# Optimization experiments

Hardware: AMD Instinct MI355X
Metric: run time of the kernel (lower is better)

## Reference

```python
import jax, jax.numpy as jnp
import numpy as np

ITER_ROUTING = 3
SIZE_IN_CAPS = 8


def squash(s, axis=-1):
    sq = jnp.sum(s * s, axis=axis, keepdims=True)
    # scale = ||s||^2 / (1 + ||s||^2); then divide by ||s|| (faithful to torch code)
    return (sq / (1.0 + sq)) * s / jnp.sqrt(sq)


def setup_inputs() -> dict:
    key = jax.random.key(0)
    k1, k2 = jax.random.split(key)
    x = jax.random.normal(k1, (256, 32, 8, 6, 6), dtype=jnp.float32)
    W = jax.random.normal(k2, (1, 10, 1152, 16, 8), dtype=jnp.float32)
    return {"x": x, "W": W}


def reference(x, W):
    B = x.shape[0]
    # torch: x.reshape(B,1,-1,8,1); W @ x -> [B,10,1152,16,1] -> squeeze
    xr = x.reshape(B, -1, SIZE_IN_CAPS)          # [B, in_caps, 8]
    u = jnp.einsum('hiws,bis->bhiw', W[0], xr)   # [B, 10, 1152, 16]
    b = jnp.zeros(u.shape[:3] + (1,), dtype=u.dtype)  # routing logits
    v = None
    for _ in range(ITER_ROUTING):
        c = jax.nn.softmax(b, axis=-2)           # softmax over in_caps
        s = jnp.sum(u * c, axis=-2)              # [B, 10, 16]
        v = squash(s, axis=-1)
        agreement = jnp.sum(u * v[:, :, None, :], axis=-1, keepdims=True)
        b = b + agreement
    return v
```

## Files before the change

### kernel.cpp

```cpp
#include <hip/hip_runtime.h>
#include <math.h>

#define NB 256
#define NH 10
#define NI 1152
#define NW 16
#define NS 8


__global__ __launch_bounds__(512, 2)
void digitcaps_kernel(const float* __restrict__ x,
                      const float* __restrict__ Wc,
                      float* __restrict__ out)
{
    __shared__ float u_lds[2][NW * NI];
    __shared__ float e_lds[2][NI];
    __shared__ float redM[8];
    __shared__ float redE[8];
    __shared__ float red3[8][16];
    __shared__ float vacc_sh[2][16];

    const int tid  = threadIdx.x;
    const int half = tid >> 8;
    const int t    = tid & 255;
    const int w    = t & 15;
    const int il   = t >> 4;
    const int lane = tid & 63;
    const int wid  = tid >> 6;

    const int blk = blockIdx.x;
    const int h   = blk >> 7;
    const int bg  = blk & 127;
    const int b   = bg * 2 + half;

    const float* xb = x  + (size_t)b * (NI * NS);
    const float* Wh = Wc + (size_t)h * ((size_t)NI * NW * NS);

    float u_reg[72];

    #pragma unroll
    for (int k = 0; k < 72; ++k) {
        int i = k * 16 + il;
        const float4* xp = reinterpret_cast<const float4*>(xb + (size_t)i * NS);
        float4 x0 = xp[0], x1 = xp[1];
        const float4* wp = reinterpret_cast<const float4*>(Wh + ((size_t)i * NW + w) * NS);
        float4 w0 = wp[0], w1 = wp[1];
        float a = w0.x*x0.x + w0.y*x0.y + w0.z*x0.z + w0.w*x0.w
                + w1.x*x1.x + w1.y*x1.y + w1.z*x1.z + w1.w*x1.w;
        u_reg[k] = a;
        u_lds[half][w * NI + (i ^ (2 * w))] = a;
    }
    if (tid < 32) vacc_sh[tid >> 4][tid & 15] = 0.0f;
    __syncthreads();

    for (int r = 0; r < 3; ++r) {
        if (r > 0) {
            float vloc[16];
            #pragma unroll
            for (int q = 0; q < 16; ++q) vloc[q] = vacc_sh[half][q];
            float dk[5];
            float m = -3.4e38f;
            #pragma unroll
            for (int k = 0; k < 5; ++k) {
                int i = t + 256 * k;
                if (k < 4 || t < (NI - 1024)) {
                    float d = 0.0f;
                    #pragma unroll
                    for (int q = 0; q < 16; ++q)
                        d += u_lds[half][q * NI + (i ^ (2 * q))] * vloc[q];
                    dk[k] = d;
                    m = fmaxf(m, d);
                }
            }
            #pragma unroll
            for (int s = 1; s < 64; s <<= 1) m = fmaxf(m, __shfl_xor(m, s));
            if (lane == 0) redM[wid] = m;
            __syncthreads();
            float M = fmaxf(fmaxf(redM[half*4+0], redM[half*4+1]),
                            fmaxf(redM[half*4+2], redM[half*4+3]));
            float Es = 0.0f;
            #pragma unroll
            for (int k = 0; k < 5; ++k) {
                int i = t + 256 * k;
                if (k < 4 || t < (NI - 1024)) {
                    float e = __expf(dk[k] - M);
                    e_lds[half][i] = e;
                    Es += e;
                }
            }
            #pragma unroll
            for (int s = 1; s < 64; s <<= 1) Es += __shfl_xor(Es, s);
            if (lane == 0) redE[wid] = Es;
            __syncthreads();
        }
        float acc = 0.0f;
        if (r == 0) {
            #pragma unroll
            for (int k = 0; k < 72; ++k) acc += u_reg[k];
        } else {
            #pragma unroll
            for (int k = 0; k < 72; ++k) acc += e_lds[half][k * 16 + il] * u_reg[k];
        }
        acc += __shfl_xor(acc, 16);
        acc += __shfl_xor(acc, 32);
        if (lane < 16) red3[wid][lane] = acc;
        __syncthreads();
        if (tid < 32) {
            int hh = tid >> 4, w2 = tid & 15;
            float s = red3[hh*4+0][w2] + red3[hh*4+1][w2]
                    + red3[hh*4+2][w2] + red3[hh*4+3][w2];
            float Eh = (r == 0) ? (float)NI
                     : (redE[hh*4+0] + redE[hh*4+1] + redE[hh*4+2] + redE[hh*4+3]);
            s /= Eh;
            float sq = s * s;
            #pragma unroll
            for (int st = 1; st < 16; st <<= 1) sq += __shfl_xor(sq, st);
            float f = sqrtf(sq) / (1.0f + sq);
            float v = s * f;
            if (r < 2) vacc_sh[hh][w2] += v;
            else {
                int bb = bg * 2 + hh;
                out[((size_t)bb * NH + h) * NW + w2] = v;
            }
        }
        __syncthreads();
    }
}

extern "C" void kernel_launch(void* const* d_in, const int* in_sizes, int n_in,
                              void* d_out, int out_size, void* d_ws, size_t ws_size,
                              hipStream_t stream) {
    const float* x  = (const float*)d_in[0];
    const float* Wc = (const float*)d_in[1];
    float* out = (float*)d_out;
    digitcaps_kernel<<<dim3(1280), dim3(512), 0, stream>>>(x, Wc, out);
}
```

Baseline: 171.8 us.

## Keep full u tile in registers with 4-lane DPP agreement and fused softmax

Each thread now holds 4 output dimensions for 18 input capsules, with one batch per 256-thread block. The agreement dot product is reduced across 4 lanes with DPP adds instead of reading a 72 KB LDS copy of u. The softmax drops max subtraction and fuses exp, normalizer and weighted sum into one pass. This removes the large shared-memory footprint, the LDS round trips and several barriers, allowing more blocks per CU. The cost is more registers per thread, and skipping max subtraction risks exp overflow for large agreement values.

```diff
diff --git a/kernel.cpp b/kernel.cpp
--- a/kernel.cpp
+++ b/kernel.cpp
@@ -1,127 +1,109 @@
 #include <hip/hip_runtime.h>
 #include <math.h>
 
-#define NB 256
 #define NH 10
 #define NI 1152
 #define NW 16
 #define NS 8
+#define NK 18
 
+template<int CTRL>
+__device__ __forceinline__ float dpp_add(float v) {
+    union { float f; int i; } a, r;
+    a.f = v;
+    r.i = __builtin_amdgcn_update_dpp(a.i, a.i, CTRL, 0xF, 0xF, true);
+    return v + r.f;
+}
 
-__global__ __launch_bounds__(512, 2)
+__global__ __launch_bounds__(256, 4)
 void digitcaps_kernel(const float* __restrict__ x,
                       const float* __restrict__ Wc,
                       float* __restrict__ out)
 {
-    __shared__ float u_lds[2][NW * NI];
-    __shared__ float e_lds[2][NI];
-    __shared__ float redM[8];
-    __shared__ float redE[8];
-    __shared__ float red3[8][16];
-    __shared__ float vacc_sh[2][16];
+    __shared__ float red3[4][NW];
+    __shared__ float redE[4];
+    __shared__ float vacc_sh[NW];
 
     const int tid  = threadIdx.x;
-    const int half = tid >> 8;
-    const int t    = tid & 255;
-    const int w    = t & 15;
-    const int il   = t >> 4;
+    const int wq   = tid & 3;
+    const int il   = tid >> 2;
     const int lane = tid & 63;
     const int wid  = tid >> 6;
 
-    const int blk = blockIdx.x;
-    const int h   = blk >> 7;
-    const int bg  = blk & 127;
-    const int b   = bg * 2 + half;
+    const int h = blockIdx.x >> 8;
+    const int b = blockIdx.x & 255;
 
     const float* xb = x  + (size_t)b * (NI * NS);
     const float* Wh = Wc + (size_t)h * ((size_t)NI * NW * NS);
 
-    float u_reg[72];
+    float u[4][NK];
 
     #pragma unroll
-    for (int k = 0; k < 72; ++k) {
-        int i = k * 16 + il;
+    for (int k = 0; k < NK; ++k) {
+        const int i = k * 64 + il;
         const float4* xp = reinterpret_cast<const float4*>(xb + (size_t)i * NS);
-        float4 x0 = xp[0], x1 = xp[1];
-        const float4* wp = reinterpret_cast<const float4*>(Wh + ((size_t)i * NW + w) * NS);
-        float4 w0 = wp[0], w1 = wp[1];
-        float a = w0.x*x0.x + w0.y*x0.y + w0.z*x0.z + w0.w*x0.w
-                + w1.x*x1.x + w1.y*x1.y + w1.z*x1.z + w1.w*x1.w;
-        u_reg[k] = a;
-        u_lds[half][w * NI + (i ^ (2 * w))] = a;
+        const float4 x0 = xp[0], x1 = xp[1];
+        #pragma unroll
+        for (int j = 0; j < 4; ++j) {
+            const float4* wp = reinterpret_cast<const float4*>(
+                Wh + ((size_t)i * NW + 4 * j + wq) * NS);
+            const float4 w0 = wp[0], w1 = wp[1];
+            u[j][k] = w0.x*x0.x + w0.y*x0.y + w0.z*x0.z + w0.w*x0.w
+                    + w1.x*x1.x + w1.y*x1.y + w1.z*x1.z + w1.w*x1.w;
+        }
     }
-    if (tid < 32) vacc_sh[tid >> 4][tid & 15] = 0.0f;
-    __syncthreads();
 
     for (int r = 0; r < 3; ++r) {
-        if (r > 0) {
-            float vloc[16];
-            #pragma unroll
-            for (int q = 0; q < 16; ++q) vloc[q] = vacc_sh[half][q];
-            float dk[5];
-            float m = -3.4e38f;
-            #pragma unroll
-            for (int k = 0; k < 5; ++k) {
-                int i = t + 256 * k;
-                if (k < 4 || t < (NI - 1024)) {
-                    float d = 0.0f;
-                    #pragma unroll
-                    for (int q = 0; q < 16; ++q)
-                        d += u_lds[half][q * NI + (i ^ (2 * q))] * vloc[q];
-                    dk[k] = d;
-                    m = fmaxf(m, d);
-                }
-            }
-            #pragma unroll
-            for (int s = 1; s < 64; s <<= 1) m = fmaxf(m, __shfl_xor(m, s));
-            if (lane == 0) redM[wid] = m;
-            __syncthreads();
-            float M = fmaxf(fmaxf(redM[half*4+0], redM[half*4+1]),
-                            fmaxf(redM[half*4+2], redM[half*4+3]));
-            float Es = 0.0f;
-            #pragma unroll
-            for (int k = 0; k < 5; ++k) {
-                int i = t + 256 * k;
-                if (k < 4 || t < (NI - 1024)) {
-                    float e = __expf(dk[k] - M);
-                    e_lds[half][i] = e;
-                    Es += e;
-                }
-            }
-            #pragma unroll
-            for (int s = 1; s < 64; s <<= 1) Es += __shfl_xor(Es, s);
-            if (lane == 0) redE[wid] = Es;
-            __syncthreads();
-        }
-        float acc = 0.0f;
+        float acc0 = 0.f, acc1 = 0.f, acc2 = 0.f, acc3 = 0.f, Ep = 0.f;
         if (r == 0) {
             #pragma unroll
-            for (int k = 0; k < 72; ++k) acc += u_reg[k];
+            for (int k = 0; k < NK; ++k) {
+                acc0 += u[0][k]; acc1 += u[1][k]; acc2 += u[2][k]; acc3 += u[3][k];
+            }
         } else {
+            const float l2e = 1.44269504088896340736f;
+            const float v0 = vacc_sh[     wq] * l2e;
+            const float v1 = vacc_sh[ 4 + wq] * l2e;
+            const float v2 = vacc_sh[ 8 + wq] * l2e;
+            const float v3 = vacc_sh[12 + wq] * l2e;
             #pragma unroll
-            for (int k = 0; k < 72; ++k) acc += e_lds[half][k * 16 + il] * u_reg[k];
+            for (int k = 0; k < NK; ++k) {
+                float p = u[0][k]*v0 + u[1][k]*v1 + u[2][k]*v2 + u[3][k]*v3;
+                p = dpp_add<0xB1>(p);
+                p = dpp_add<0x4E>(p);
+                const float e = exp2f(p);
+                Ep += e;
+                acc0 += e * u[0][k]; acc1 += e * u[1][k];
+                acc2 += e * u[2][k]; acc3 += e * u[3][k];
+            }
         }
-        acc += __shfl_xor(acc, 16);
-        acc += __shfl_xor(acc, 32);
-        if (lane < 16) red3[wid][lane] = acc;
+        #pragma unroll
+        for (int s = 4; s < 64; s <<= 1) {
+            acc0 += __shfl_xor(acc0, s); acc1 += __shfl_xor(acc1, s);
+            acc2 += __shfl_xor(acc2, s); acc3 += __shfl_xor(acc3, s);
+            Ep   += __shfl_xor(Ep, s);
+        }
+        if (lane < 4) {
+            red3[wid][ 0 + lane] = acc0;
+            red3[wid][ 4 + lane] = acc1;
+            red3[wid][ 8 + lane] = acc2;
+            red3[wid][12 + lane] = acc3;
+            if (lane == 0) redE[wid] = Ep;
+        }
         __syncthreads();
-        if (tid < 32) {
-            int hh = tid >> 4, w2 = tid & 15;
-            float s = red3[hh*4+0][w2] + red3[hh*4+1][w2]
-                    + red3[hh*4+2][w2] + red3[hh*4+3][w2];
-            float Eh = (r == 0) ? (float)NI
-                     : (redE[hh*4+0] + redE[hh*4+1] + redE[hh*4+2] + redE[hh*4+3]);
-            s /= Eh;
+        if (tid < NW) {
+            float s = red3[0][tid] + red3[1][tid] + red3[2][tid] + red3[3][tid];
+            const float E = (r == 0) ? (float)NI
+                                     : (redE[0] + redE[1] + redE[2] + redE[3]);
+            s /= E;
             float sq = s * s;
             #pragma unroll
             for (int st = 1; st < 16; st <<= 1) sq += __shfl_xor(sq, st);
-            float f = sqrtf(sq) / (1.0f + sq);
-            float v = s * f;
-            if (r < 2) vacc_sh[hh][w2] += v;
-            else {
-                int bb = bg * 2 + hh;
-                out[((size_t)bb * NH + h) * NW + w2] = v;
-            }
+            const float f = sqrtf(sq) / (1.0f + sq);
+            const float v = s * f;
+            if      (r == 0) vacc_sh[tid]  = v;
+            else if (r == 1) vacc_sh[tid] += v;
+            else out[((size_t)b * NH + h) * NW + tid] = v;
         }
         __syncthreads();
     }
@@ -133,5 +115,5 @@
     const float* x  = (const float*)d_in[0];
     const float* Wc = (const float*)d_in[1];
     float* out = (float*)d_out;
-    digitcaps_kernel<<<dim3(1280), dim3(512), 0, stream>>>(x, Wc, out);
+    digitcaps_kernel<<<dim3(NH * 256), dim3(256), 0, stream>>>(x, Wc, out);
 }
```

After: 155.5 us. -9.5%, faster.
